# Kernel tuning notes

Measured on AMD Instinct MI355X. Metric: run time of the kernel, lower is better.

The kernel has to match this reference:

```python
import jax, jax.numpy as jnp
import numpy as np

LOG2 = float(np.log(2.0))
CUTOFF = 10.0
INPUT_DIM = 5


def ssp(x):
    # ShiftedSoftplus
    return jax.nn.softplus(x) - LOG2


def setup_inputs() -> dict:
    key = jax.random.key(0)
    ks = jax.random.split(key, 16)
    N, E, D, G, L = 20000, 320000, 128, 100, 6
    s = 0.05
    return {
        "z": jax.random.normal(ks[0], (N, INPUT_DIM + D), jnp.float32),
        "edge_index": jax.random.randint(ks[1], (2, E), 0, N, dtype=jnp.int64),
        "edge_length": jax.random.uniform(ks[2], (E,), jnp.float32),
        "edge_attr": jax.random.uniform(ks[3], (E, G), jnp.float32),
        "emblin_w": jax.random.normal(ks[4], (D, INPUT_DIM), jnp.float32) * s,
        "emblin_b": jnp.zeros((D,), jnp.float32),
        "mlp_w1": jax.random.normal(ks[5], (L, D, G), jnp.float32) * s,
        "mlp_b1": jnp.zeros((L, D), jnp.float32),
        "mlp_w2": jax.random.normal(ks[6], (L, D, D), jnp.float32) * s,
        "mlp_b2": jnp.zeros((L, D), jnp.float32),
        "lin1_w": jax.random.normal(ks[7], (L, D, D), jnp.float32) * s,
        "lin2_w": jax.random.normal(ks[8], (L, D, D), jnp.float32) * s,
        "lin2_b": jnp.zeros((L, D), jnp.float32),
        "lin_w": jax.random.normal(ks[9], (L, D, 2 * D), jnp.float32) * s,
        "lin_b": jnp.zeros((L, D), jnp.float32),
    }


def reference(z, edge_index, edge_length, edge_attr, emblin_w, emblin_b,
              mlp_w1, mlp_b1, mlp_w2, mlp_b2, lin1_w, lin2_w, lin2_b,
              lin_w, lin_b):
    # time_emb=True path: split z into node features and time embedding
    zf, ptemb = z[:, :INPUT_DIM], z[:, INPUT_DIM:]
    h = zf @ emblin_w.T + emblin_b + ptemb          # [N, D]
    src, dst = edge_index[0], edge_index[1]
    N = h.shape[0]
    # non-smooth cutoff gate: C = (edge_length <= cutoff)
    C = (edge_length <= CUTOFF).astype(h.dtype)     # [E]
    L = mlp_w1.shape[0]
    for l in range(L):
        # edge-wise filter MLP with cutoff gate
        Wf = ssp(edge_attr @ mlp_w1[l].T + mlp_b1[l]) @ mlp_w2[l].T + mlp_b2[l]
        Wf = Wf * C[:, None]                        # [E, F]
        xf = h @ lin1_w[l].T                        # [N, F]
        m_ij = xf[src] * Wf                         # gather + elementwise, [E, F]
        m_i = jax.ops.segment_sum(m_ij, dst, num_segments=N)  # scatter-add, [N, F]
        m = ssp(m_i @ lin2_w[l].T + lin2_b[l])      # [N, D]
        h = h + (jnp.concatenate([h, m], axis=1) @ lin_w[l].T + lin_b[l])
    return h
```

## Files before the change

### kernel.cpp

```cpp
#include <hip/hip_runtime.h>

#define N_NODES 20000
#define D 128
#define E_EDGES 320000
#define G 100
#define L_LAYERS 6
#define IN_DIM 5
#define ZROW (IN_DIM + D)
#define CUTOFF_V 10.0f
#define LOG2F_ 0.69314718055994530942f

typedef __attribute__((ext_vector_type(8))) short bf16x8;
typedef __attribute__((ext_vector_type(4))) float f32x4;
typedef unsigned short ushort_t;
typedef unsigned int uint_t;

__device__ __forceinline__ float sspf(float x) {
    return fmaxf(x, 0.0f) + __logf(1.0f + __expf(-fabsf(x))) - LOG2F_;
}

__device__ __forceinline__ ushort_t f2bf(float f) {
    union { float f; uint_t u; } x; x.f = f;
    uint_t r = ((x.u >> 16) & 1u) + 0x7fffu;
    return (ushort_t)((x.u + r) >> 16);
}

__device__ __forceinline__ uint_t pack2(float a, float b) {
    return (uint_t)f2bf(a) | ((uint_t)f2bf(b) << 16);
}

__device__ __forceinline__ f32x4 mfma_bf16(bf16x8 a, bf16x8 b, f32x4 c) {
    return __builtin_amdgcn_mfma_f32_16x16x32_bf16(a, b, c, 0, 0, 0);
}

__global__ void embed_kernel(const float* __restrict__ z,
                             const float* __restrict__ ew,
                             const float* __restrict__ eb,
                             float* __restrict__ h) {
    int n = blockIdx.x;
    int d = threadIdx.x;
    const float* zr = z + (size_t)n * ZROW;
    float acc = eb[d] + zr[IN_DIM + d];
#pragma unroll
    for (int k = 0; k < IN_DIM; ++k) acc += zr[k] * ew[d * IN_DIM + k];
    h[(size_t)n * D + d] = acc;
}

__global__ void convw1_kernel(const float* __restrict__ w1, ushort_t* __restrict__ out) {
    int idx = blockIdx.x * 256 + threadIdx.x;
    int k = idx & 127;
    int nl = idx >> 7;
    out[idx] = (k < G) ? f2bf(w1[(size_t)nl * G + k]) : (ushort_t)0;
}

__global__ void castbf_kernel(const float* __restrict__ src, ushort_t* __restrict__ dst) {
    int i = blockIdx.x * 256 + threadIdx.x;
    dst[i] = f2bf(src[i]);
}

__global__ void hist_kernel(const int* __restrict__ ei, int* __restrict__ deg) {
    int e = blockIdx.x * 256 + threadIdx.x;
    atomicAdd(&deg[ei[E_EDGES + e]], 1);
}

__global__ __launch_bounds__(1024) void scan_kernel(const int* __restrict__ deg,
                                                    int* __restrict__ row_start,
                                                    int* __restrict__ cursor) {
    __shared__ int wsum[16];
    int t = threadIdx.x;
    const int CH = (N_NODES + 1023) / 1024;
    int base = t * CH;
    int s = 0;
    for (int i = 0; i < CH; ++i) {
        int idx = base + i;
        if (idx < N_NODES) s += deg[idx];
    }
    int lane = t & 63, wid = t >> 6;
    int v = s;
    for (int o = 1; o < 64; o <<= 1) {
        int u = __shfl_up(v, o, 64);
        if (lane >= o) v += u;
    }
    if (lane == 63) wsum[wid] = v;
    __syncthreads();
    if (t == 0) {
        int acc = 0;
        for (int i = 0; i < 16; ++i) { int tmp = wsum[i]; wsum[i] = acc; acc += tmp; }
    }
    __syncthreads();
    int run = v - s + wsum[wid];
    for (int i = 0; i < CH; ++i) {
        int idx = base + i;
        if (idx < N_NODES) {
            row_start[idx] = run;
            cursor[idx] = run;
            run += deg[idx];
        }
    }
    if (t == 0) row_start[N_NODES] = E_EDGES;
}

__global__ void scatter_perm_kernel(const int* __restrict__ ei, int* __restrict__ cursor,
                                    int* __restrict__ perm, int* __restrict__ src_p) {
    int e = blockIdx.x * 256 + threadIdx.x;
    int d = ei[E_EDGES + e];
    int p = atomicAdd(&cursor[d], 1);
    perm[p] = e;
    src_p[p] = ei[e];
}

__global__ __launch_bounds__(256) void edge_mlp_kernel(
    const float* __restrict__ edge_attr, const float* __restrict__ el,
    const int* __restrict__ perm,
    const ushort_t* __restrict__ w1b, const float* __restrict__ b1,
    const ushort_t* __restrict__ w2b, const float* __restrict__ b2,
    ushort_t* __restrict__ wf) {
    __shared__ __align__(16) ushort_t sT[128][136];
    __shared__ int s_pe[128];
    __shared__ float s_cm[128];

    int t = threadIdx.x, lane = t & 63, wid = t >> 6;
    int c = lane & 15, quad = lane >> 4;
    int e0 = blockIdx.x * 128, rbase = wid * 32;

    if (lane < 32) {
        int pe = perm[e0 + rbase + lane];
        s_pe[rbase + lane] = pe;
        s_cm[rbase + lane] = (el[pe] <= CUTOFF_V) ? 1.0f : 0.0f;
    }
#pragma unroll
    for (int i = 0; i < 16; ++i) {
        int idx = i * 64 + lane;
        int r = idx >> 5, ch = idx & 31;
        float4 v = make_float4(0.f, 0.f, 0.f, 0.f);
        if (ch < 25) {
            int pe = s_pe[rbase + r];
            v = *(const float4*)(edge_attr + (size_t)pe * G + ch * 4);
        }
        uint2 p; p.x = pack2(v.x, v.y); p.y = pack2(v.z, v.w);
        *(uint2*)(&sT[rbase + r][ch * 4]) = p;
    }

    f32x4 acc[2][8];
#pragma unroll
    for (int st = 0; st < 2; ++st)
#pragma unroll
        for (int ct = 0; ct < 8; ++ct) acc[st][ct] = (f32x4){0.f, 0.f, 0.f, 0.f};

#pragma unroll
    for (int ks = 0; ks < 4; ++ks) {
        int koff = ks * 32 + quad * 8;
        bf16x8 b0 = *(const bf16x8*)(&sT[rbase + c][koff]);
        bf16x8 b1v = *(const bf16x8*)(&sT[rbase + 16 + c][koff]);
#pragma unroll
        for (int ct = 0; ct < 8; ++ct) {
            bf16x8 a = *(const bf16x8*)(w1b + (size_t)(ct * 16 + c) * 128 + koff);
            acc[0][ct] = mfma_bf16(a, b0, acc[0][ct]);
            acc[1][ct] = mfma_bf16(a, b1v, acc[1][ct]);
        }
    }
#pragma unroll
    for (int st = 0; st < 2; ++st)
#pragma unroll
        for (int ct = 0; ct < 8; ++ct) {
            int col = ct * 16 + quad * 4;
            float4 bv = *(const float4*)(b1 + col);
            uint2 p;
            p.x = pack2(sspf(acc[st][ct][0] + bv.x), sspf(acc[st][ct][1] + bv.y));
            p.y = pack2(sspf(acc[st][ct][2] + bv.z), sspf(acc[st][ct][3] + bv.w));
            *(uint2*)(&sT[rbase + st * 16 + c][col]) = p;
        }

#pragma unroll
    for (int st = 0; st < 2; ++st)
#pragma unroll
        for (int ct = 0; ct < 8; ++ct) acc[st][ct] = (f32x4){0.f, 0.f, 0.f, 0.f};
#pragma unroll
    for (int ks = 0; ks < 4; ++ks) {
        int koff = ks * 32 + quad * 8;
        bf16x8 b0 = *(const bf16x8*)(&sT[rbase + c][koff]);
        bf16x8 b1v = *(const bf16x8*)(&sT[rbase + 16 + c][koff]);
#pragma unroll
        for (int ct = 0; ct < 8; ++ct) {
            bf16x8 a = *(const bf16x8*)(w2b + (size_t)(ct * 16 + c) * 128 + koff);
            acc[0][ct] = mfma_bf16(a, b0, acc[0][ct]);
            acc[1][ct] = mfma_bf16(a, b1v, acc[1][ct]);
        }
    }
#pragma unroll
    for (int st = 0; st < 2; ++st) {
        int e = e0 + rbase + st * 16 + c;
        float cv = s_cm[rbase + st * 16 + c];
#pragma unroll
        for (int ct = 0; ct < 8; ++ct) {
            int col = ct * 16 + quad * 4;
            float4 bv = *(const float4*)(b2 + col);
            uint2 p;
            p.x = pack2((acc[st][ct][0] + bv.x) * cv, (acc[st][ct][1] + bv.y) * cv);
            p.y = pack2((acc[st][ct][2] + bv.z) * cv, (acc[st][ct][3] + bv.w) * cv);
            *(uint2*)(wf + (size_t)e * 128 + col) = p;
        }
    }
}

template <bool HASB, bool SSP, bool RES, bool BF16OUT, bool TWOK>
__global__ __launch_bounds__(256) void node_mfma_kernel(
    const float* __restrict__ in0, const float* __restrict__ in1,
    const ushort_t* __restrict__ Wb, const float* __restrict__ bias,
    const float* __restrict__ resid, void* __restrict__ outp) {
    __shared__ __align__(16) ushort_t sT[128][136];
    const int WS = TWOK ? 256 : 128;
    int t = threadIdx.x, lane = t & 63, wid = t >> 6;
    int c = lane & 15, quad = lane >> 4;
    int n0 = blockIdx.x * 128, rbase = wid * 32;

    f32x4 acc[2][8];
#pragma unroll
    for (int st = 0; st < 2; ++st)
#pragma unroll
        for (int ct = 0; ct < 8; ++ct) acc[st][ct] = (f32x4){0.f, 0.f, 0.f, 0.f};

    const float* src = in0;
#pragma unroll 1
    for (int ph = 0; ph < (TWOK ? 2 : 1); ++ph) {
#pragma unroll
        for (int i = 0; i < 16; ++i) {
            int idx = i * 64 + lane;
            int r = idx >> 5, ch = idx & 31;
            int gr = n0 + rbase + r;
            float4 v = make_float4(0.f, 0.f, 0.f, 0.f);
            if (gr < N_NODES) v = *(const float4*)(src + (size_t)gr * 128 + ch * 4);
            uint2 p; p.x = pack2(v.x, v.y); p.y = pack2(v.z, v.w);
            *(uint2*)(&sT[rbase + r][ch * 4]) = p;
        }
        int kb = ph * 128;
#pragma unroll
        for (int ks = 0; ks < 4; ++ks) {
            int koff = ks * 32 + quad * 8;
            bf16x8 b0 = *(const bf16x8*)(&sT[rbase + c][koff]);
            bf16x8 b1v = *(const bf16x8*)(&sT[rbase + 16 + c][koff]);
#pragma unroll
            for (int ct = 0; ct < 8; ++ct) {
                bf16x8 a = *(const bf16x8*)(Wb + (size_t)(ct * 16 + c) * WS + kb + koff);
                acc[0][ct] = mfma_bf16(a, b0, acc[0][ct]);
                acc[1][ct] = mfma_bf16(a, b1v, acc[1][ct]);
            }
        }
        src = in1;
    }

#pragma unroll
    for (int st = 0; st < 2; ++st) {
        int node = n0 + rbase + st * 16 + c;
        if (node < N_NODES) {
#pragma unroll
            for (int ct = 0; ct < 8; ++ct) {
                int col = ct * 16 + quad * 4;
                float4 bv = make_float4(0.f, 0.f, 0.f, 0.f);
                if (HASB) bv = *(const float4*)(bias + col);
                float v0 = acc[st][ct][0] + bv.x;
                float v1 = acc[st][ct][1] + bv.y;
                float v2 = acc[st][ct][2] + bv.z;
                float v3 = acc[st][ct][3] + bv.w;
                if (SSP) { v0 = sspf(v0); v1 = sspf(v1); v2 = sspf(v2); v3 = sspf(v3); }
                if (RES) {
                    float4 rv = *(const float4*)(resid + (size_t)node * 128 + col);
                    v0 += rv.x; v1 += rv.y; v2 += rv.z; v3 += rv.w;
                }
                if (BF16OUT) {
                    uint2 p; p.x = pack2(v0, v1); p.y = pack2(v2, v3);
                    *(uint2*)((ushort_t*)outp + (size_t)node * 128 + col) = p;
                } else {
                    *(float4*)((float*)outp + (size_t)node * 128 + col) =
                        make_float4(v0, v1, v2, v3);
                }
            }
        }
    }
}

__global__ __launch_bounds__(256) void segsum_kernel(
    const ushort_t* __restrict__ wf, const ushort_t* __restrict__ xf_bf,
    const int* __restrict__ row_start, const int* __restrict__ src_p,
    float* __restrict__ m_i) {
    int t = threadIdx.x, lane = t & 63;
    int n = blockIdx.x * 4 + (t >> 6);
    int beg = row_start[n], end = row_start[n + 1];
    float a0 = 0.f, a1 = 0.f;
    for (int i = beg; i < end; ++i) {
        uint_t w = *(const uint_t*)(wf + (size_t)i * 128 + lane * 2);
        uint_t x = *(const uint_t*)(xf_bf + (size_t)src_p[i] * 128 + lane * 2);
        a0 += __uint_as_float(w << 16) * __uint_as_float(x << 16);
        a1 += __uint_as_float(w & 0xffff0000u) * __uint_as_float(x & 0xffff0000u);
    }
    *(float2*)(m_i + (size_t)n * 128 + lane * 2) = make_float2(a0, a1);
}

extern "C" void kernel_launch(void* const* d_in, const int* in_sizes, int n_in,
                              void* d_out, int out_size, void* d_ws, size_t ws_size,
                              hipStream_t stream) {
    const float* z        = (const float*)d_in[0];
    const int*   ei       = (const int*)d_in[1];
    const float* el       = (const float*)d_in[2];
    const float* ea       = (const float*)d_in[3];
    const float* emblin_w = (const float*)d_in[4];
    const float* emblin_b = (const float*)d_in[5];
    const float* mlp_w1   = (const float*)d_in[6];
    const float* mlp_b1   = (const float*)d_in[7];
    const float* mlp_w2   = (const float*)d_in[8];
    const float* mlp_b2   = (const float*)d_in[9];
    const float* lin1_w   = (const float*)d_in[10];
    const float* lin2_w   = (const float*)d_in[11];
    const float* lin2_b   = (const float*)d_in[12];
    const float* lin_w    = (const float*)d_in[13];
    const float* lin_b    = (const float*)d_in[14];
    (void)in_sizes; (void)n_in; (void)out_size; (void)ws_size;

    const size_t ND = (size_t)N_NODES * D;
    float* ws   = (float*)d_ws;
    float* h    = ws;
    float* m_i  = h + ND;
    float* fend = m_i + ND;

    ushort_t* w1b   = (ushort_t*)fend;
    ushort_t* w2b   = w1b   + (size_t)L_LAYERS * D * 128;
    ushort_t* lin1b = w2b   + (size_t)L_LAYERS * D * D;
    ushort_t* lin2b = lin1b + (size_t)L_LAYERS * D * D;
    ushort_t* linwb = lin2b + (size_t)L_LAYERS * D * D;
    ushort_t* wf    = linwb + (size_t)L_LAYERS * D * 256;
    ushort_t* xf_bf = wf    + (size_t)E_EDGES * 128;
    int* ibase      = (int*)(xf_bf + ND);
    int* deg        = ibase;
    int* row_start  = deg + N_NODES;
    int* cursor     = row_start + N_NODES + 1;
    int* perm       = cursor + N_NODES;
    int* src_p      = perm + E_EDGES;

    convw1_kernel<<<(L_LAYERS * D * 128) / 256, 256, 0, stream>>>(mlp_w1, w1b);
    castbf_kernel<<<(L_LAYERS * D * D) / 256, 256, 0, stream>>>(mlp_w2, w2b);
    castbf_kernel<<<(L_LAYERS * D * D) / 256, 256, 0, stream>>>(lin1_w, lin1b);
    castbf_kernel<<<(L_LAYERS * D * D) / 256, 256, 0, stream>>>(lin2_w, lin2b);
    castbf_kernel<<<(L_LAYERS * D * 256) / 256, 256, 0, stream>>>(lin_w, linwb);

    hipMemsetAsync(deg, 0, (size_t)N_NODES * sizeof(int), stream);
    hist_kernel<<<E_EDGES / 256, 256, 0, stream>>>(ei, deg);
    scan_kernel<<<1, 1024, 0, stream>>>(deg, row_start, cursor);
    scatter_perm_kernel<<<E_EDGES / 256, 256, 0, stream>>>(ei, cursor, perm, src_p);

    embed_kernel<<<N_NODES, D, 0, stream>>>(z, emblin_w, emblin_b, h);

    const int NBLK = (N_NODES + 127) / 128;
    for (int l = 0; l < L_LAYERS; ++l) {
        node_mfma_kernel<false, false, false, true, false><<<NBLK, 256, 0, stream>>>(
            h, nullptr, lin1b + (size_t)l * D * D, nullptr, nullptr, xf_bf);
        edge_mlp_kernel<<<E_EDGES / 128, 256, 0, stream>>>(
            ea, el, perm, w1b + (size_t)l * D * 128, mlp_b1 + (size_t)l * D,
            w2b + (size_t)l * D * D, mlp_b2 + (size_t)l * D, wf);
        segsum_kernel<<<N_NODES / 4, 256, 0, stream>>>(wf, xf_bf, row_start, src_p, m_i);
        node_mfma_kernel<true, true, false, false, false><<<NBLK, 256, 0, stream>>>(
            m_i, nullptr, lin2b + (size_t)l * D * D, lin2_b + (size_t)l * D,
            nullptr, m_i);
        node_mfma_kernel<true, false, true, false, true><<<NBLK, 256, 0, stream>>>(
            h, m_i, linwb + (size_t)l * D * 256, lin_b + (size_t)l * D, h, h);
    }

    hipMemcpyAsync(d_out, h, ND * sizeof(float), hipMemcpyDeviceToDevice, stream);
}
```

Measured before the change: 1.619 ms.

## Pre-pack permuted edge attributes once, slim edge MLP, fuse node update GEMMs

The permuted gather of edge_attr and the cutoff mask are hoisted out of the layer loop. They are computed once into a contiguous bf16 buffer and a mask array, so the six per-layer edge MLPs read sequential, already-packed data instead of doing a random fp32 gather. The edge MLP now uses 64-edge blocks with per-wave register B fragments and a smaller shared tile, with launch bounds set for higher occupancy. The lin2+ssp and concat-linear+residual node GEMMs are fused into one kernel, which removes a round trip of m_i through global memory and one launch per layer. The cost is extra workspace for the bf16 attribute copy and mask.

Result: slower. 2.029 ms (+25.4%).

```diff
diff --git a/kernel.cpp b/kernel.cpp
--- a/kernel.cpp
+++ b/kernel.cpp
@@ -109,97 +109,83 @@
     src_p[p] = ei[e];
 }
 
-__global__ __launch_bounds__(256) void edge_mlp_kernel(
-    const float* __restrict__ edge_attr, const float* __restrict__ el,
-    const int* __restrict__ perm,
+__global__ void attr_prep_kernel(const float* __restrict__ ea,
+                                 const int* __restrict__ perm,
+                                 ushort_t* __restrict__ attr_bf) {
+    int t = threadIdx.x;
+    int half = t >> 5;
+    int ch = t & 31;
+    int r = blockIdx.x * 8 + half;
+    int pe = perm[r];
+    float4 v = make_float4(0.f, 0.f, 0.f, 0.f);
+    if (ch < 25) v = *(const float4*)(ea + (size_t)pe * G + ch * 4);
+    uint2 p; p.x = pack2(v.x, v.y); p.y = pack2(v.z, v.w);
+    *(uint2*)(attr_bf + (size_t)r * 128 + ch * 4) = p;
+}
+
+__global__ void cmask_kernel(const float* __restrict__ el, const int* __restrict__ perm,
+                             float* __restrict__ c_mask) {
+    int e = blockIdx.x * 256 + threadIdx.x;
+    c_mask[e] = (el[perm[e]] <= CUTOFF_V) ? 1.0f : 0.0f;
+}
+
+__global__ __launch_bounds__(256, 8) void edge_mlp_kernel(
+    const ushort_t* __restrict__ attr_bf, const float* __restrict__ c_mask,
     const ushort_t* __restrict__ w1b, const float* __restrict__ b1,
     const ushort_t* __restrict__ w2b, const float* __restrict__ b2,
     ushort_t* __restrict__ wf) {
-    __shared__ __align__(16) ushort_t sT[128][136];
-    __shared__ int s_pe[128];
-    __shared__ float s_cm[128];
+    __shared__ __align__(16) ushort_t sU[64][136];
 
     int t = threadIdx.x, lane = t & 63, wid = t >> 6;
     int c = lane & 15, quad = lane >> 4;
-    int e0 = blockIdx.x * 128, rbase = wid * 32;
-
-    if (lane < 32) {
-        int pe = perm[e0 + rbase + lane];
-        s_pe[rbase + lane] = pe;
-        s_cm[rbase + lane] = (el[pe] <= CUTOFF_V) ? 1.0f : 0.0f;
-    }
-#pragma unroll
-    for (int i = 0; i < 16; ++i) {
-        int idx = i * 64 + lane;
-        int r = idx >> 5, ch = idx & 31;
-        float4 v = make_float4(0.f, 0.f, 0.f, 0.f);
-        if (ch < 25) {
-            int pe = s_pe[rbase + r];
-            v = *(const float4*)(edge_attr + (size_t)pe * G + ch * 4);
-        }
-        uint2 p; p.x = pack2(v.x, v.y); p.y = pack2(v.z, v.w);
-        *(uint2*)(&sT[rbase + r][ch * 4]) = p;
-    }
-
-    f32x4 acc[2][8];
-#pragma unroll
-    for (int st = 0; st < 2; ++st)
-#pragma unroll
-        for (int ct = 0; ct < 8; ++ct) acc[st][ct] = (f32x4){0.f, 0.f, 0.f, 0.f};
-
-#pragma unroll
-    for (int ks = 0; ks < 4; ++ks) {
-        int koff = ks * 32 + quad * 8;
-        bf16x8 b0 = *(const bf16x8*)(&sT[rbase + c][koff]);
-        bf16x8 b1v = *(const bf16x8*)(&sT[rbase + 16 + c][koff]);
-#pragma unroll
-        for (int ct = 0; ct < 8; ++ct) {
-            bf16x8 a = *(const bf16x8*)(w1b + (size_t)(ct * 16 + c) * 128 + koff);
-            acc[0][ct] = mfma_bf16(a, b0, acc[0][ct]);
-            acc[1][ct] = mfma_bf16(a, b1v, acc[1][ct]);
-        }
-    }
-#pragma unroll
-    for (int st = 0; st < 2; ++st)
-#pragma unroll
-        for (int ct = 0; ct < 8; ++ct) {
-            int col = ct * 16 + quad * 4;
-            float4 bv = *(const float4*)(b1 + col);
-            uint2 p;
-            p.x = pack2(sspf(acc[st][ct][0] + bv.x), sspf(acc[st][ct][1] + bv.y));
-            p.y = pack2(sspf(acc[st][ct][2] + bv.z), sspf(acc[st][ct][3] + bv.w));
-            *(uint2*)(&sT[rbase + st * 16 + c][col]) = p;
-        }
-
-#pragma unroll
-    for (int st = 0; st < 2; ++st)
-#pragma unroll
-        for (int ct = 0; ct < 8; ++ct) acc[st][ct] = (f32x4){0.f, 0.f, 0.f, 0.f};
-#pragma unroll
-    for (int ks = 0; ks < 4; ++ks) {
-        int koff = ks * 32 + quad * 8;
-        bf16x8 b0 = *(const bf16x8*)(&sT[rbase + c][koff]);
-        bf16x8 b1v = *(const bf16x8*)(&sT[rbase + 16 + c][koff]);
-#pragma unroll
-        for (int ct = 0; ct < 8; ++ct) {
-            bf16x8 a = *(const bf16x8*)(w2b + (size_t)(ct * 16 + c) * 128 + koff);
-            acc[0][ct] = mfma_bf16(a, b0, acc[0][ct]);
-            acc[1][ct] = mfma_bf16(a, b1v, acc[1][ct]);
-        }
-    }
-#pragma unroll
-    for (int st = 0; st < 2; ++st) {
-        int e = e0 + rbase + st * 16 + c;
-        float cv = s_cm[rbase + st * 16 + c];
-#pragma unroll
-        for (int ct = 0; ct < 8; ++ct) {
-            int col = ct * 16 + quad * 4;
-            float4 bv = *(const float4*)(b2 + col);
-            uint2 p;
-            p.x = pack2((acc[st][ct][0] + bv.x) * cv, (acc[st][ct][1] + bv.y) * cv);
-            p.y = pack2((acc[st][ct][2] + bv.z) * cv, (acc[st][ct][3] + bv.w) * cv);
-            *(uint2*)(wf + (size_t)e * 128 + col) = p;
-        }
+    int e0 = blockIdx.x * 64, rbase = wid * 16;
+    int erow = e0 + rbase + c;
+
+    bf16x8 b[4];
+#pragma unroll
+    for (int ks = 0; ks < 4; ++ks)
+        b[ks] = *(const bf16x8*)(attr_bf + (size_t)erow * 128 + ks * 32 + quad * 8);
+    f32x4 acc[8];
+#pragma unroll
+    for (int i = 0; i < 8; ++i) acc[i] = (f32x4){0.f, 0.f, 0.f, 0.f};
+#pragma unroll
+    for (int ct = 0; ct < 8; ++ct)
+#pragma unroll
+        for (int ks = 0; ks < 4; ++ks) {
+            bf16x8 a = *(const bf16x8*)(w1b + (size_t)(ct * 16 + c) * 128 + ks * 32 + quad * 8);
+            acc[ct] = mfma_bf16(a, b[ks], acc[ct]);
+        }
+#pragma unroll
+    for (int ct = 0; ct < 8; ++ct) {
+        int col = ct * 16 + quad * 4;
+        float4 bv = *(const float4*)(b1 + col);
+        uint2 p;
+        p.x = pack2(sspf(acc[ct][0] + bv.x), sspf(acc[ct][1] + bv.y));
+        p.y = pack2(sspf(acc[ct][2] + bv.z), sspf(acc[ct][3] + bv.w));
+        *(uint2*)(&sU[rbase + c][col]) = p;
+    }
+
+#pragma unroll
+    for (int ks = 0; ks < 4; ++ks)
+        b[ks] = *(const bf16x8*)(&sU[rbase + c][ks * 32 + quad * 8]);
+#pragma unroll
+    for (int i = 0; i < 8; ++i) acc[i] = (f32x4){0.f, 0.f, 0.f, 0.f};
+#pragma unroll
+    for (int ct = 0; ct < 8; ++ct)
+#pragma unroll
+        for (int ks = 0; ks < 4; ++ks) {
+            bf16x8 a = *(const bf16x8*)(w2b + (size_t)(ct * 16 + c) * 128 + ks * 32 + quad * 8);
+            acc[ct] = mfma_bf16(a, b[ks], acc[ct]);
+        }
+    float cv = c_mask[erow];
+#pragma unroll
+    for (int ct = 0; ct < 8; ++ct) {
+        int col = ct * 16 + quad * 4;
+        float4 bv = *(const float4*)(b2 + col);
+        uint2 p;
+        p.x = pack2((acc[ct][0] + bv.x) * cv, (acc[ct][1] + bv.y) * cv);
+        p.y = pack2((acc[ct][2] + bv.z) * cv, (acc[ct][3] + bv.w) * cv);
+        *(uint2*)(wf + (size_t)erow * 128 + col) = p;
     }
 }
 
@@ -279,6 +265,98 @@
     }
 }
 
+__global__ __launch_bounds__(256, 8) void update_fused_kernel(
+    float* __restrict__ h, const float* __restrict__ m_i,
+    const ushort_t* __restrict__ lin2b, const float* __restrict__ lin2_b,
+    const ushort_t* __restrict__ linwb, const float* __restrict__ lin_b) {
+    __shared__ __align__(16) ushort_t sM[64][136];
+    int t = threadIdx.x, lane = t & 63, wid = t >> 6;
+    int c = lane & 15, quad = lane >> 4;
+    int n0 = blockIdx.x * 64, rbase = wid * 16;
+
+#pragma unroll
+    for (int i = 0; i < 8; ++i) {
+        int idx = i * 64 + lane;
+        int r = idx >> 5, ch = idx & 31;
+        int gr = n0 + rbase + r;
+        float4 v = make_float4(0.f, 0.f, 0.f, 0.f);
+        if (gr < N_NODES) v = *(const float4*)(m_i + (size_t)gr * 128 + ch * 4);
+        uint2 p; p.x = pack2(v.x, v.y); p.y = pack2(v.z, v.w);
+        *(uint2*)(&sM[rbase + r][ch * 4]) = p;
+    }
+
+    bf16x8 b[4];
+#pragma unroll
+    for (int ks = 0; ks < 4; ++ks)
+        b[ks] = *(const bf16x8*)(&sM[rbase + c][ks * 32 + quad * 8]);
+    f32x4 acc[8];
+#pragma unroll
+    for (int i = 0; i < 8; ++i) acc[i] = (f32x4){0.f, 0.f, 0.f, 0.f};
+#pragma unroll
+    for (int ct = 0; ct < 8; ++ct)
+#pragma unroll
+        for (int ks = 0; ks < 4; ++ks) {
+            bf16x8 a = *(const bf16x8*)(lin2b + (size_t)(ct * 16 + c) * 128 + ks * 32 + quad * 8);
+            acc[ct] = mfma_bf16(a, b[ks], acc[ct]);
+        }
+#pragma unroll
+    for (int ct = 0; ct < 8; ++ct) {
+        int col = ct * 16 + quad * 4;
+        float4 bv = *(const float4*)(lin2_b + col);
+        uint2 p;
+        p.x = pack2(sspf(acc[ct][0] + bv.x), sspf(acc[ct][1] + bv.y));
+        p.y = pack2(sspf(acc[ct][2] + bv.z), sspf(acc[ct][3] + bv.w));
+        *(uint2*)(&sM[rbase + c][col]) = p;
+    }
+
+#pragma unroll
+    for (int ks = 0; ks < 4; ++ks)
+        b[ks] = *(const bf16x8*)(&sM[rbase + c][ks * 32 + quad * 8]);
+#pragma unroll
+    for (int i = 0; i < 8; ++i) acc[i] = (f32x4){0.f, 0.f, 0.f, 0.f};
+#pragma unroll
+    for (int ct = 0; ct < 8; ++ct)
+#pragma unroll
+        for (int ks = 0; ks < 4; ++ks) {
+            bf16x8 a = *(const bf16x8*)(linwb + (size_t)(ct * 16 + c) * 256 + 128 + ks * 32 + quad * 8);
+            acc[ct] = mfma_bf16(a, b[ks], acc[ct]);
+        }
+
+    int gr = n0 + rbase + c;
+#pragma unroll
+    for (int ks = 0; ks < 4; ++ks) {
+        float4 v0 = make_float4(0.f, 0.f, 0.f, 0.f), v1 = v0;
+        if (gr < N_NODES) {
+            const float* hp = h + (size_t)gr * 128 + ks * 32 + quad * 8;
+            v0 = *(const float4*)(hp);
+            v1 = *(const float4*)(hp + 4);
+        }
+        union { bf16x8 v; uint4 u; } hb;
+        hb.u.x = pack2(v0.x, v0.y); hb.u.y = pack2(v0.z, v0.w);
+        hb.u.z = pack2(v1.x, v1.y); hb.u.w = pack2(v1.z, v1.w);
+        b[ks] = hb.v;
+    }
+#pragma unroll
+    for (int ct = 0; ct < 8; ++ct)
+#pragma unroll
+        for (int ks = 0; ks < 4; ++ks) {
+            bf16x8 a = *(const bf16x8*)(linwb + (size_t)(ct * 16 + c) * 256 + ks * 32 + quad * 8);
+            acc[ct] = mfma_bf16(a, b[ks], acc[ct]);
+        }
+
+    if (gr < N_NODES) {
+#pragma unroll
+        for (int ct = 0; ct < 8; ++ct) {
+            int col = ct * 16 + quad * 4;
+            float4 bv = *(const float4*)(lin_b + col);
+            float4 hv = *(const float4*)(h + (size_t)gr * 128 + col);
+            *(float4*)(h + (size_t)gr * 128 + col) = make_float4(
+                hv.x + acc[ct][0] + bv.x, hv.y + acc[ct][1] + bv.y,
+                hv.z + acc[ct][2] + bv.z, hv.w + acc[ct][3] + bv.w);
+        }
+    }
+}
+
 __global__ __launch_bounds__(256) void segsum_kernel(
     const ushort_t* __restrict__ wf, const ushort_t* __restrict__ xf_bf,
     const int* __restrict__ row_start, const int* __restrict__ src_p,
@@ -320,16 +398,18 @@
     float* ws   = (float*)d_ws;
     float* h    = ws;
     float* m_i  = h + ND;
-    float* fend = m_i + ND;
-
-    ushort_t* w1b   = (ushort_t*)fend;
-    ushort_t* w2b   = w1b   + (size_t)L_LAYERS * D * 128;
-    ushort_t* lin1b = w2b   + (size_t)L_LAYERS * D * D;
-    ushort_t* lin2b = lin1b + (size_t)L_LAYERS * D * D;
-    ushort_t* linwb = lin2b + (size_t)L_LAYERS * D * D;
-    ushort_t* wf    = linwb + (size_t)L_LAYERS * D * 256;
-    ushort_t* xf_bf = wf    + (size_t)E_EDGES * 128;
-    int* ibase      = (int*)(xf_bf + ND);
+    float* c_mask = m_i + ND;
+    float* fend = c_mask + E_EDGES;
+
+    ushort_t* w1b     = (ushort_t*)fend;
+    ushort_t* w2b     = w1b   + (size_t)L_LAYERS * D * 128;
+    ushort_t* lin1b   = w2b   + (size_t)L_LAYERS * D * D;
+    ushort_t* lin2b   = lin1b + (size_t)L_LAYERS * D * D;
+    ushort_t* linwb   = lin2b + (size_t)L_LAYERS * D * D;
+    ushort_t* wf      = linwb + (size_t)L_LAYERS * D * 256;
+    ushort_t* xf_bf   = wf    + (size_t)E_EDGES * 128;
+    ushort_t* attr_bf = xf_bf + ND;
+    int* ibase      = (int*)(attr_bf + (size_t)E_EDGES * 128);
     int* deg        = ibase;
     int* row_start  = deg + N_NODES;
     int* cursor     = row_start + N_NODES + 1;
@@ -346,22 +426,23 @@
     hist_kernel<<<E_EDGES / 256, 256, 0, stream>>>(ei, deg);
     scan_kernel<<<1, 1024, 0, stream>>>(deg, row_start, cursor);
     scatter_perm_kernel<<<E_EDGES / 256, 256, 0, stream>>>(ei, cursor, perm, src_p);
+    attr_prep_kernel<<<E_EDGES / 8, 256, 0, stream>>>(ea, perm, attr_bf);
+    cmask_kernel<<<E_EDGES / 256, 256, 0, stream>>>(el, perm, c_mask);
 
     embed_kernel<<<N_NODES, D, 0, stream>>>(z, emblin_w, emblin_b, h);
 
     const int NBLK = (N_NODES + 127) / 128;
+    const int UBLK = (N_NODES + 63) / 64;
     for (int l = 0; l < L_LAYERS; ++l) {
         node_mfma_kernel<false, false, false, true, false><<<NBLK, 256, 0, stream>>>(
             h, nullptr, lin1b + (size_t)l * D * D, nullptr, nullptr, xf_bf);
-        edge_mlp_kernel<<<E_EDGES / 128, 256, 0, stream>>>(
-            ea, el, perm, w1b + (size_t)l * D * 128, mlp_b1 + (size_t)l * D,
+        edge_mlp_kernel<<<E_EDGES / 64, 256, 0, stream>>>(
+            attr_bf, c_mask, w1b + (size_t)l * D * 128, mlp_b1 + (size_t)l * D,
             w2b + (size_t)l * D * D, mlp_b2 + (size_t)l * D, wf);
         segsum_kernel<<<N_NODES / 4, 256, 0, stream>>>(wf, xf_bf, row_start, src_p, m_i);
-        node_mfma_kernel<true, true, false, false, false><<<NBLK, 256, 0, stream>>>(
-            m_i, nullptr, lin2b + (size_t)l * D * D, lin2_b + (size_t)l * D,
-            nullptr, m_i);
-        node_mfma_kernel<true, false, true, false, true><<<NBLK, 256, 0, stream>>>(
-            h, m_i, linwb + (size_t)l * D * 256, lin_b + (size_t)l * D, h, h);
+        update_fused_kernel<<<UBLK, 256, 0, stream>>>(
+            h, m_i, lin2b + (size_t)l * D * D, lin2_b + (size_t)l * D,
+            linwb + (size_t)l * D * 256, lin_b + (size_t)l * D);
     }
 
     hipMemcpyAsync(d_out, h, ND * sizeof(float), hipMemcpyDeviceToDevice, stream);
```
